# Kernel optimization log

Measured on AMD Instinct MI355X. Metric: run time of the kernel, lower is better.

The kernel has to match this reference:

```python
import jax, jax.numpy as jnp
import numpy as np


def gcn_layer(x, src, dst, deg_inv_sqrt, W, b):
    # PyG GCNConv: h = X W; out[i] = sum_{j->i} norm(j,i) * h[j] + deg_i^{-1} * h[i] + b
    n = x.shape[0]
    h = x @ W                                   # [N, out]
    norm = deg_inv_sqrt[src] * deg_inv_sqrt[dst]  # [E]
    msg = h[src] * norm[:, None]                # [E, out]
    agg = jax.ops.segment_sum(msg, dst, num_segments=n)
    # self-loop contribution (added loops with norm = deg_i^{-1})
    agg = agg + h * (deg_inv_sqrt * deg_inv_sqrt)[:, None]
    return agg + b


def setup_inputs() -> dict:
    key = jax.random.key(0)
    k1, k2, k3, k4, k5, k6 = jax.random.split(key, 6)
    N, E, IN, HID, OUT = 50000, 800000, 128, 128, 64
    x = jax.random.normal(k1, (N, IN), dtype=jnp.float32)
    edge_index = jax.random.randint(k2, (2, E), 0, N, dtype=jnp.int64)
    # glorot-ish init for weights, zeros-ish bias
    W1 = jax.random.normal(k3, (IN, HID), dtype=jnp.float32) * (1.0 / np.sqrt(IN))
    b1 = jax.random.normal(k4, (HID,), dtype=jnp.float32) * 0.01
    W2 = jax.random.normal(k5, (HID, OUT), dtype=jnp.float32) * (1.0 / np.sqrt(HID))
    b2 = jax.random.normal(k6, (OUT,), dtype=jnp.float32) * 0.01
    return {"x": x, "edge_index": edge_index, "W1": W1, "b1": b1, "W2": W2, "b2": b2}


def reference(x, edge_index, W1, b1, W2, b2):
    n = x.shape[0]
    src, dst = edge_index[0], edge_index[1]
    # degree with self-loops (PyG computes degree on the dst/col index)
    deg = jax.ops.segment_sum(jnp.ones_like(dst, dtype=x.dtype), dst, num_segments=n) + 1.0
    deg_inv_sqrt = jax.lax.rsqrt(deg)
    h = gcn_layer(x, src, dst, deg_inv_sqrt, W1, b1)
    h = jax.nn.relu(h)
    # F.dropout with training=False is identity (module evaluated in eval mode)
    out = gcn_layer(h, src, dst, deg_inv_sqrt, W2, b2)
    return out
```

## Files before the change

### kernel.cpp

```cpp
#include <hip/hip_runtime.h>
#include <stdint.h>

typedef __attribute__((ext_vector_type(8))) short short8;
typedef __attribute__((ext_vector_type(4))) float floatx4;

static inline size_t align256(size_t x) { return (x + 255) & ~size_t(255); }

__device__ __forceinline__ unsigned short f2bf(float f) {
    unsigned u = __float_as_uint(f);
    u += 0x7fff + ((u >> 16) & 1);
    return (unsigned short)(u >> 16);
}
__device__ __forceinline__ unsigned pack_bf16(float a, float b) {
    return (unsigned)f2bf(a) | ((unsigned)f2bf(b) << 16);
}
__device__ __forceinline__ float bf_lo(unsigned u) { return __uint_as_float(u << 16); }
__device__ __forceinline__ float bf_hi(unsigned u) { return __uint_as_float(u & 0xffff0000u); }

#define BSHIFT 7
#define NBMAX 1024
#define CH 2048
#define SCAP 3072

__device__ __forceinline__ bool detect_i32(const void* eidx, int E, int t) {
    const long long* e64 = (const long long*)eidx;
    int nchk = E < 256 ? E : 256;
    long long v = e64[t % nchk];
    int bad = (v < 0 || v > 0x7fffffffLL) ? 1 : 0;
    return __syncthreads_or(bad) != 0;
}

__global__ __launch_bounds__(256) void k_hist(const void* __restrict__ eidx, int E,
        int* __restrict__ chist, int NB, int NC,
        const float* __restrict__ W1, const float* __restrict__ W2,
        unsigned short* __restrict__ w1t, unsigned short* __restrict__ w2t,
        int K1, int M1, int K2, int M2) {
    __shared__ int hist[NBMAX];
    const int t = threadIdx.x, B = blockIdx.x;
    if (B < NC) {
        const int e0 = B * CH;
        const int e1 = (e0 + CH < E) ? e0 + CH : E;
        const bool i32 = detect_i32(eidx, E, t);
        const int* e32 = (const int*)eidx;
        const long long* e64 = (const long long*)eidx;
        for (int b0 = 0; b0 < NB; b0 += NBMAX) {
            int bw = (NB - b0 < NBMAX) ? NB - b0 : NBMAX;
            for (int i = t; i < bw; i += 256) hist[i] = 0;
            __syncthreads();
            for (int e = e0 + t; e < e1; e += 256) {
                int d = i32 ? e32[(size_t)E + e] : (int)e64[(size_t)E + e];
                int b = (d >> BSHIFT) - b0;
                if (b >= 0 && b < bw) atomicAdd(&hist[b], 1);
            }
            __syncthreads();
            for (int i = t; i < bw; i += 256) chist[(size_t)(b0 + i) * NC + B] = hist[i];
            __syncthreads();
        }
    } else if (B == NC) {
        for (int j = t; j < K1 * M1; j += 256) {
            int k = j / M1, n = j % M1;
            w1t[(size_t)n * K1 + k] = f2bf(W1[j]);
        }
    } else if (B == NC + 1) {
        for (int j = t; j < K2 * M2; j += 256) {
            int k = j / M2, n = j % M2;
            w2t[(size_t)n * K2 + k] = f2bf(W2[j]);
        }
    }
}

__global__ __launch_bounds__(256) void k_btot(const int* __restrict__ chist,
                                              int* __restrict__ btot, int NB, int NC) {
    int b = blockIdx.x * 4 + (threadIdx.x >> 6);
    if (b >= NB) return;
    int lane = threadIdx.x & 63;
    const int* row = chist + (size_t)b * NC;
    int v = 0;
    for (int i = lane; i < NC; i += 64) v += row[i];
    #pragma unroll
    for (int off = 32; off >= 1; off >>= 1) v += __shfl_xor(v, off, 64);
    if (lane == 0) btot[b] = v;
}

__global__ __launch_bounds__(1024) void k_bscan(const int* __restrict__ btot,
                                                int* __restrict__ bbase,
                                                int* __restrict__ rs_final,
                                                int NB, int N) {
    __shared__ int swt[16];
    const int t = threadIdx.x, lane = t & 63, w = t >> 6;
    int carry = 0;
    for (int base = 0; base < NB; base += 1024) {
        int i = base + t;
        int v = (i < NB) ? btot[i] : 0;
        int incl = v;
        #pragma unroll
        for (int off = 1; off < 64; off <<= 1) {
            int nbr = __shfl_up(incl, off, 64);
            if (lane >= off) incl += nbr;
        }
        if (lane == 63) swt[w] = incl;
        __syncthreads();
        int woff = 0;
        for (int j = 0; j < w; ++j) woff += swt[j];
        if (i < NB) bbase[i] = carry + woff + incl - v;
        int tot = 0;
        for (int j = 0; j < 16; ++j) tot += swt[j];
        carry += tot;
        __syncthreads();
    }
    if (t == 0) { bbase[NB] = carry; rs_final[N] = carry; }
}

__global__ __launch_bounds__(256) void k_hscan2(int* __restrict__ chist,
                                                const int* __restrict__ bbase,
                                                int NB, int NC) {
    int b = blockIdx.x * 4 + (threadIdx.x >> 6);
    if (b >= NB) return;
    int lane = threadIdx.x & 63;
    int* row = chist + (size_t)b * NC;
    int carry = bbase[b];
    for (int base = 0; base < NC; base += 64) {
        int i = base + lane;
        int v = (i < NC) ? row[i] : 0;
        int incl = v;
        #pragma unroll
        for (int off = 1; off < 64; off <<= 1) {
            int nbr = __shfl_up(incl, off, 64);
            if (lane >= off) incl += nbr;
        }
        if (i < NC) row[i] = carry + incl - v;
        carry += __shfl(incl, 63, 64);
    }
}

__global__ __launch_bounds__(256) void k_bfill(const void* __restrict__ eidx, int E,
                                               const int* __restrict__ chist,
                                               uint2* __restrict__ bbuf, int NB, int NC) {
    __shared__ int rank[NBMAX];
    __shared__ int base[NBMAX];
    const int t = threadIdx.x, c = blockIdx.x;
    const int e0 = c * CH;
    const int e1 = (e0 + CH < E) ? e0 + CH : E;
    const bool i32 = detect_i32(eidx, E, t);
    const int* e32 = (const int*)eidx;
    const long long* e64 = (const long long*)eidx;
    for (int b0 = 0; b0 < NB; b0 += NBMAX) {
        int bw = (NB - b0 < NBMAX) ? NB - b0 : NBMAX;
        for (int i = t; i < bw; i += 256) {
            rank[i] = 0;
            base[i] = chist[(size_t)(b0 + i) * NC + c];
        }
        __syncthreads();
        for (int e = e0 + t; e < e1; e += 256) {
            int s, d;
            if (i32) { s = e32[e]; d = e32[(size_t)E + e]; }
            else     { s = (int)e64[e]; d = (int)e64[(size_t)E + e]; }
            int b = (d >> BSHIFT) - b0;
            if (b >= 0 && b < bw) {
                int slot = base[b] + atomicAdd(&rank[b], 1);
                bbuf[slot] = make_uint2((unsigned)s, (unsigned)d);
            }
        }
        __syncthreads();
    }
}

__global__ __launch_bounds__(256) void k_sort(const uint2* __restrict__ bbuf,
                                              const int* __restrict__ bbase,
                                              int* __restrict__ rs_final,
                                              float* __restrict__ dinv,
                                              int* __restrict__ esrc, int N) {
    __shared__ int hist[128];
    __shared__ int off[128];
    __shared__ int srcbuf[SCAP];
    const int b = blockIdx.x, t = threadIdx.x;
    const int node0 = b << BSHIFT;
    const int nloc = (N - node0 < 128) ? N - node0 : 128;
    const int s0 = bbase[b], s1 = bbase[b + 1];
    const int cnt = s1 - s0;
    if (t < 128) hist[t] = 0;
    __syncthreads();
    for (int i = s0 + t; i < s1; i += 256)
        atomicAdd(&hist[bbuf[i].y - (unsigned)node0], 1);
    __syncthreads();
    if (t < 64) {
        int carry = 0;
        #pragma unroll
        for (int base = 0; base < 128; base += 64) {
            int v = hist[base + t];
            int incl = v;
            #pragma unroll
            for (int o = 1; o < 64; o <<= 1) {
                int nbr = __shfl_up(incl, o, 64);
                if (t >= o) incl += nbr;
            }
            off[base + t] = carry + incl - v;
            carry += __shfl(incl, 63, 64);
        }
    }
    __syncthreads();
    if (t < nloc) {
        rs_final[node0 + t] = s0 + off[t];
        dinv[node0 + t] = rsqrtf((float)hist[t] + 1.0f);
    }
    __syncthreads();
    if (t < 128) hist[t] = 0;
    __syncthreads();
    if (cnt <= SCAP) {
        for (int i = s0 + t; i < s1; i += 256) {
            uint2 sd = bbuf[i];
            int lo = sd.y - (unsigned)node0;
            int r = atomicAdd(&hist[lo], 1);
            srcbuf[off[lo] + r] = (int)sd.x;
        }
        __syncthreads();
        for (int i = t; i < cnt; i += 256) esrc[s0 + i] = srcbuf[i];
    } else {
        for (int i = s0 + t; i < s1; i += 256) {
            uint2 sd = bbuf[i];
            int lo = sd.y - (unsigned)node0;
            int r = atomicAdd(&hist[lo], 1);
            esrc[s0 + off[lo] + r] = (int)sd.x;
        }
    }
}

template<int BN, bool AF32>
__global__ __launch_bounds__(256, 3) void k_gemm(
        const void* __restrict__ Av, const unsigned short* __restrict__ Bt,
        const float* __restrict__ dinv, unsigned short* __restrict__ C,
        int N, int M) {
    constexpr int LD = 136;
    __shared__ unsigned short As[64 * LD];
    __shared__ unsigned short Bs[BN * LD];
    const int tid = threadIdx.x;
    const int wave = tid >> 6, lane = tid & 63;
    const int q = lane >> 4, tm = lane & 15;
    const int row0 = blockIdx.x * 64;

    {
        const uint4* Bg = (const uint4*)Bt;
        #pragma unroll
        for (int it = 0; it < BN / 16; ++it) {
            int i = tid + it * 256;
            int r = i >> 4, o = i & 15;
            *(uint4*)&Bs[r * LD + o * 8] = Bg[(size_t)r * 16 + o];
        }
    }
    if (AF32) {
        const float4* Ag = (const float4*)Av;
        #pragma unroll
        for (int it = 0; it < 8; ++it) {
            int i = tid + it * 256;
            int r = i >> 5, o = i & 31;
            int row = row0 + r;
            float4 v = make_float4(0.f, 0.f, 0.f, 0.f);
            if (row < N) v = Ag[(size_t)row * 32 + o];
            uint2 pk;
            pk.x = pack_bf16(v.x, v.y);
            pk.y = pack_bf16(v.z, v.w);
            *(uint2*)&As[r * LD + o * 4] = pk;
        }
    } else {
        const uint4* Ag = (const uint4*)Av;
        #pragma unroll
        for (int it = 0; it < 4; ++it) {
            int i = tid + it * 256;
            int r = i >> 4, o = i & 15;
            int row = row0 + r;
            uint4 v = make_uint4(0, 0, 0, 0);
            if (row < N) v = Ag[(size_t)row * 16 + o];
            *(uint4*)&As[r * LD + o * 8] = v;
        }
    }
    __syncthreads();

    constexpr int NG = BN / 16;
    floatx4 acc[NG];
    #pragma unroll
    for (int g = 0; g < NG; ++g) acc[g] = (floatx4){0.f, 0.f, 0.f, 0.f};

    const int arow = wave * 16 + tm;
    #pragma unroll
    for (int kc = 0; kc < 4; ++kc) {
        short8 af = *(const short8*)&As[arow * LD + kc * 32 + q * 8];
        #pragma unroll
        for (int g = 0; g < NG; ++g) {
            short8 bf = *(const short8*)&Bs[(g * 16 + tm) * LD + kc * 32 + q * 8];
            acc[g] = __builtin_amdgcn_mfma_f32_16x16x32_bf16(af, bf, acc[g], 0, 0, 0);
        }
    }

    float dv[4];
    #pragma unroll
    for (int r = 0; r < 4; ++r) {
        int row = row0 + wave * 16 + q * 4 + r;
        dv[r] = (row < N) ? dinv[row] : 0.f;
    }
    #pragma unroll
    for (int g = 0; g < NG; ++g) {
        #pragma unroll
        for (int r = 0; r < 4; ++r) {
            int row = row0 + wave * 16 + q * 4 + r;
            if (row < N) C[(size_t)row * M + g * 16 + tm] = f2bf(dv[r] * acc[g][r]);
        }
    }
}

__global__ __launch_bounds__(256) void k_agg128(const unsigned* __restrict__ Hb,
        const float* __restrict__ dinv, const int* __restrict__ rs,
        const int* __restrict__ esrc, const float* __restrict__ bias,
        unsigned* __restrict__ out, int N) {
    int wid = (blockIdx.x * 256 + threadIdx.x) >> 6;
    if (wid >= N) return;
    int l = threadIdx.x & 63;
    float di = dinv[wid];
    unsigned a = Hb[(size_t)wid * 64 + l];
    float accx = bf_lo(a), accy = bf_hi(a);
    int k = rs[wid], kend = rs[wid + 1];
    for (; k + 8 <= kend; k += 8) {
        int s[8];
        #pragma unroll
        for (int j = 0; j < 8; ++j) s[j] = esrc[k + j];
        unsigned g[8];
        #pragma unroll
        for (int j = 0; j < 8; ++j) g[j] = Hb[(size_t)s[j] * 64 + l];
        #pragma unroll
        for (int j = 0; j < 8; ++j) { accx += bf_lo(g[j]); accy += bf_hi(g[j]); }
    }
    if (k + 4 <= kend) {
        int s[4];
        #pragma unroll
        for (int j = 0; j < 4; ++j) s[j] = esrc[k + j];
        unsigned g[4];
        #pragma unroll
        for (int j = 0; j < 4; ++j) g[j] = Hb[(size_t)s[j] * 64 + l];
        #pragma unroll
        for (int j = 0; j < 4; ++j) { accx += bf_lo(g[j]); accy += bf_hi(g[j]); }
        k += 4;
    }
    for (; k < kend; ++k) {
        unsigned g = Hb[(size_t)esrc[k] * 64 + l];
        accx += bf_lo(g); accy += bf_hi(g);
    }
    float2 b = ((const float2*)bias)[l];
    float ox = fmaxf(fmaf(di, accx, b.x), 0.f);
    float oy = fmaxf(fmaf(di, accy, b.y), 0.f);
    out[(size_t)wid * 64 + l] = pack_bf16(ox, oy);
}

__global__ __launch_bounds__(256) void k_agg64(const unsigned short* __restrict__ Hb,
        const float* __restrict__ dinv, const int* __restrict__ rs,
        const int* __restrict__ esrc, const float* __restrict__ bias,
        float* __restrict__ out, int N) {
    int wid = (blockIdx.x * 256 + threadIdx.x) >> 6;
    if (wid >= N) return;
    int l = threadIdx.x & 63;
    float di = dinv[wid];
    float acc = __uint_as_float((unsigned)Hb[(size_t)wid * 64 + l] << 16);
    int k = rs[wid], kend = rs[wid + 1];
    for (; k + 8 <= kend; k += 8) {
        int s[8];
        #pragma unroll
        for (int j = 0; j < 8; ++j) s[j] = esrc[k + j];
        unsigned short g[8];
        #pragma unroll
        for (int j = 0; j < 8; ++j) g[j] = Hb[(size_t)s[j] * 64 + l];
        #pragma unroll
        for (int j = 0; j < 8; ++j) acc += __uint_as_float((unsigned)g[j] << 16);
    }
    if (k + 4 <= kend) {
        int s[4];
        #pragma unroll
        for (int j = 0; j < 4; ++j) s[j] = esrc[k + j];
        unsigned short g[4];
        #pragma unroll
        for (int j = 0; j < 4; ++j) g[j] = Hb[(size_t)s[j] * 64 + l];
        #pragma unroll
        for (int j = 0; j < 4; ++j) acc += __uint_as_float((unsigned)g[j] << 16);
        k += 4;
    }
    for (; k < kend; ++k)
        acc += __uint_as_float((unsigned)Hb[(size_t)esrc[k] * 64 + l] << 16);
    out[(size_t)wid * 64 + l] = fmaf(di, acc, bias[l]);
}

extern "C" void kernel_launch(void* const* d_in, const int* in_sizes, int n_in,
                              void* d_out, int out_size, void* d_ws, size_t ws_size,
                              hipStream_t stream) {
    const float* x  = (const float*)d_in[0];
    const void*  ei = d_in[1];
    const float* W1 = (const float*)d_in[2];
    const float* b1 = (const float*)d_in[3];
    const float* W2 = (const float*)d_in[4];
    const float* b2 = (const float*)d_in[5];

    int HID = in_sizes[3];
    int IN  = in_sizes[2] / HID;
    int OUT = in_sizes[4] / HID;
    int N   = in_sizes[0] / IN;
    int E   = in_sizes[1] / 2;
    int NB  = (N + 127) >> BSHIFT;
    int NC  = (E + CH - 1) / CH;

    char* p = (char*)d_ws;
    int* chist     = (int*)p;   p += align256((size_t)NB * NC * 4);
    int* btot      = (int*)p;   p += align256((size_t)NB * 4);
    int* bbase     = (int*)p;   p += align256((size_t)(NB + 1) * 4);
    int* rs_final  = (int*)p;   p += align256((size_t)(N + 1) * 4);
    int* esrc      = (int*)p;   p += align256((size_t)E * 4);
    float* dinv    = (float*)p; p += align256((size_t)N * 4);
    unsigned short* w1t = (unsigned short*)p; p += align256((size_t)HID * IN * 2);
    unsigned short* w2t = (unsigned short*)p; p += align256((size_t)OUT * HID * 2);
    size_t hb_bytes = (size_t)N * HID * 2, bbuf_bytes = (size_t)E * 8;
    uint2* bbuf    = (uint2*)p;
    unsigned short* hb = (unsigned short*)p;
    p += align256(hb_bytes > bbuf_bytes ? hb_bytes : bbuf_bytes);
    unsigned short* h1b = (unsigned short*)p; p += align256((size_t)N * HID * 2);
    unsigned short* h2b = (unsigned short*)p; p += align256((size_t)N * OUT * 2);

    k_hist<<<NC + 2, 256, 0, stream>>>(ei, E, chist, NB, NC,
                                       W1, W2, w1t, w2t, IN, HID, HID, OUT);
    k_btot<<<(NB + 3) / 4, 256, 0, stream>>>(chist, btot, NB, NC);
    k_bscan<<<1, 1024, 0, stream>>>(btot, bbase, rs_final, NB, N);
    k_hscan2<<<(NB + 3) / 4, 256, 0, stream>>>(chist, bbase, NB, NC);
    k_bfill<<<NC, 256, 0, stream>>>(ei, E, chist, bbuf, NB, NC);
    k_sort<<<NB, 256, 0, stream>>>(bbuf, bbase, rs_final, dinv, esrc, N);

    k_gemm<128, true><<<(N + 63) / 64, 256, 0, stream>>>(x, w1t, dinv, hb, N, HID);
    k_agg128<<<(N + 3) / 4, 256, 0, stream>>>((unsigned*)hb, dinv, rs_final, esrc, b1,
                                              (unsigned*)h1b, N);

    k_gemm<64, false><<<(N + 63) / 64, 256, 0, stream>>>(h1b, w2t, dinv, h2b, N, OUT);
    k_agg64<<<(N + 3) / 4, 256, 0, stream>>>(h2b, dinv, rs_final, esrc, b2, (float*)d_out, N);
}
```

Baseline: 208.1 us.

## Split wave into edge sub-groups with 16-byte gathers and fuse block-total scan

The aggregation kernels now split each 64-lane wave into sub-groups that each handle a different edge. Every lane gathers a uint4 of bf16 features, and the partial sums are reduced across sub-groups with xor shuffles. This replaces per-lane 4-byte and 2-byte gathers with 16-byte loads, so more edges are in flight per wave and fewer, wider memory requests are issued. The block-total kernel is also folded into the single-block scan, which removes one launch but serialises the histogram row sums onto one workgroup. The shuffle reduction and masked tail handling add ALU work, and the fused scan assumes NB <= 1024.

```diff
diff --git a/kernel.cpp b/kernel.cpp
--- a/kernel.cpp
+++ b/kernel.cpp
@@ -69,46 +69,39 @@
     }
 }
 
-__global__ __launch_bounds__(256) void k_btot(const int* __restrict__ chist,
-                                              int* __restrict__ btot, int NB, int NC) {
-    int b = blockIdx.x * 4 + (threadIdx.x >> 6);
-    if (b >= NB) return;
-    int lane = threadIdx.x & 63;
-    const int* row = chist + (size_t)b * NC;
-    int v = 0;
-    for (int i = lane; i < NC; i += 64) v += row[i];
-    #pragma unroll
-    for (int off = 32; off >= 1; off >>= 1) v += __shfl_xor(v, off, 64);
-    if (lane == 0) btot[b] = v;
-}
-
-__global__ __launch_bounds__(1024) void k_bscan(const int* __restrict__ btot,
+__global__ __launch_bounds__(1024) void k_bscan(const int* __restrict__ chist,
                                                 int* __restrict__ bbase,
                                                 int* __restrict__ rs_final,
-                                                int NB, int N) {
+                                                int NB, int NC, int N) {
+    __shared__ int tot[1024];
     __shared__ int swt[16];
     const int t = threadIdx.x, lane = t & 63, w = t >> 6;
-    int carry = 0;
-    for (int base = 0; base < NB; base += 1024) {
-        int i = base + t;
-        int v = (i < NB) ? btot[i] : 0;
-        int incl = v;
-        #pragma unroll
-        for (int off = 1; off < 64; off <<= 1) {
-            int nbr = __shfl_up(incl, off, 64);
-            if (lane >= off) incl += nbr;
-        }
-        if (lane == 63) swt[w] = incl;
-        __syncthreads();
-        int woff = 0;
-        for (int j = 0; j < w; ++j) woff += swt[j];
-        if (i < NB) bbase[i] = carry + woff + incl - v;
-        int tot = 0;
-        for (int j = 0; j < 16; ++j) tot += swt[j];
-        carry += tot;
-        __syncthreads();
-    }
-    if (t == 0) { bbase[NB] = carry; rs_final[N] = carry; }
+    for (int b = w; b < NB; b += 16) {
+        const int* row = chist + (size_t)b * NC;
+        int v = 0;
+        for (int i = lane; i < NC; i += 64) v += row[i];
+        #pragma unroll
+        for (int off = 32; off >= 1; off >>= 1) v += __shfl_xor(v, off, 64);
+        if (lane == 0) tot[b] = v;
+    }
+    __syncthreads();
+    int v = (t < NB) ? tot[t] : 0;
+    int incl = v;
+    #pragma unroll
+    for (int off = 1; off < 64; off <<= 1) {
+        int nbr = __shfl_up(incl, off, 64);
+        if (lane >= off) incl += nbr;
+    }
+    if (lane == 63) swt[w] = incl;
+    __syncthreads();
+    int woff = 0;
+    for (int j = 0; j < w; ++j) woff += swt[j];
+    if (t < NB) bbase[t] = woff + incl - v;
+    if (t == 1023) {
+        int total = woff + incl;
+        bbase[NB] = total;
+        rs_final[N] = total;
+    }
 }
 
 __global__ __launch_bounds__(256) void k_hscan2(int* __restrict__ chist,
@@ -307,82 +300,139 @@
     }
 }
 
-__global__ __launch_bounds__(256) void k_agg128(const unsigned* __restrict__ Hb,
+__global__ __launch_bounds__(256) void k_agg128(const uint4* __restrict__ Hv,
         const float* __restrict__ dinv, const int* __restrict__ rs,
         const int* __restrict__ esrc, const float* __restrict__ bias,
-        unsigned* __restrict__ out, int N) {
+        uint4* __restrict__ out, int N) {
     int wid = (blockIdx.x * 256 + threadIdx.x) >> 6;
     if (wid >= N) return;
-    int l = threadIdx.x & 63;
-    float di = dinv[wid];
-    unsigned a = Hb[(size_t)wid * 64 + l];
-    float accx = bf_lo(a), accy = bf_hi(a);
+    const int l = threadIdx.x & 63;
+    const int sub = l >> 4, fl = l & 15;
+    float acc[8];
+    {
+        uint4 a = Hv[(size_t)wid * 16 + fl];
+        float m = (sub == 0) ? 1.f : 0.f;
+        acc[0] = m * bf_lo(a.x); acc[1] = m * bf_hi(a.x);
+        acc[2] = m * bf_lo(a.y); acc[3] = m * bf_hi(a.y);
+        acc[4] = m * bf_lo(a.z); acc[5] = m * bf_hi(a.z);
+        acc[6] = m * bf_lo(a.w); acc[7] = m * bf_hi(a.w);
+    }
     int k = rs[wid], kend = rs[wid + 1];
     for (; k + 8 <= kend; k += 8) {
-        int s[8];
-        #pragma unroll
-        for (int j = 0; j < 8; ++j) s[j] = esrc[k + j];
-        unsigned g[8];
-        #pragma unroll
-        for (int j = 0; j < 8; ++j) g[j] = Hb[(size_t)s[j] * 64 + l];
-        #pragma unroll
-        for (int j = 0; j < 8; ++j) { accx += bf_lo(g[j]); accy += bf_hi(g[j]); }
-    }
-    if (k + 4 <= kend) {
-        int s[4];
-        #pragma unroll
-        for (int j = 0; j < 4; ++j) s[j] = esrc[k + j];
-        unsigned g[4];
-        #pragma unroll
-        for (int j = 0; j < 4; ++j) g[j] = Hb[(size_t)s[j] * 64 + l];
-        #pragma unroll
-        for (int j = 0; j < 4; ++j) { accx += bf_lo(g[j]); accy += bf_hi(g[j]); }
-        k += 4;
-    }
-    for (; k < kend; ++k) {
-        unsigned g = Hb[(size_t)esrc[k] * 64 + l];
-        accx += bf_lo(g); accy += bf_hi(g);
-    }
-    float2 b = ((const float2*)bias)[l];
-    float ox = fmaxf(fmaf(di, accx, b.x), 0.f);
-    float oy = fmaxf(fmaf(di, accy, b.y), 0.f);
-    out[(size_t)wid * 64 + l] = pack_bf16(ox, oy);
-}
-
-__global__ __launch_bounds__(256) void k_agg64(const unsigned short* __restrict__ Hb,
+        int sA = esrc[k + sub];
+        int sB = esrc[k + 4 + sub];
+        uint4 gA = Hv[(size_t)sA * 16 + fl];
+        uint4 gB = Hv[(size_t)sB * 16 + fl];
+        acc[0] += bf_lo(gA.x); acc[1] += bf_hi(gA.x);
+        acc[2] += bf_lo(gA.y); acc[3] += bf_hi(gA.y);
+        acc[4] += bf_lo(gA.z); acc[5] += bf_hi(gA.z);
+        acc[6] += bf_lo(gA.w); acc[7] += bf_hi(gA.w);
+        acc[0] += bf_lo(gB.x); acc[1] += bf_hi(gB.x);
+        acc[2] += bf_lo(gB.y); acc[3] += bf_hi(gB.y);
+        acc[4] += bf_lo(gB.z); acc[5] += bf_hi(gB.z);
+        acc[6] += bf_lo(gB.w); acc[7] += bf_hi(gB.w);
+    }
+    if (k < kend) {
+        int e1 = k + sub, e2 = k + 4 + sub;
+        bool v1 = e1 < kend, v2 = e2 < kend;
+        int sA = v1 ? esrc[e1] : wid;
+        int sB = v2 ? esrc[e2] : wid;
+        uint4 gA = Hv[(size_t)sA * 16 + fl];
+        uint4 gB = Hv[(size_t)sB * 16 + fl];
+        float m1 = v1 ? 1.f : 0.f, m2 = v2 ? 1.f : 0.f;
+        acc[0] = fmaf(m1, bf_lo(gA.x), acc[0]); acc[1] = fmaf(m1, bf_hi(gA.x), acc[1]);
+        acc[2] = fmaf(m1, bf_lo(gA.y), acc[2]); acc[3] = fmaf(m1, bf_hi(gA.y), acc[3]);
+        acc[4] = fmaf(m1, bf_lo(gA.z), acc[4]); acc[5] = fmaf(m1, bf_hi(gA.z), acc[5]);
+        acc[6] = fmaf(m1, bf_lo(gA.w), acc[6]); acc[7] = fmaf(m1, bf_hi(gA.w), acc[7]);
+        acc[0] = fmaf(m2, bf_lo(gB.x), acc[0]); acc[1] = fmaf(m2, bf_hi(gB.x), acc[1]);
+        acc[2] = fmaf(m2, bf_lo(gB.y), acc[2]); acc[3] = fmaf(m2, bf_hi(gB.y), acc[3]);
+        acc[4] = fmaf(m2, bf_lo(gB.z), acc[4]); acc[5] = fmaf(m2, bf_hi(gB.z), acc[5]);
+        acc[6] = fmaf(m2, bf_lo(gB.w), acc[6]); acc[7] = fmaf(m2, bf_hi(gB.w), acc[7]);
+    }
+    #pragma unroll
+    for (int j = 0; j < 8; ++j) {
+        acc[j] += __shfl_xor(acc[j], 16, 64);
+        acc[j] += __shfl_xor(acc[j], 32, 64);
+    }
+    if (sub == 0) {
+        float di = dinv[wid];
+        float4 b0 = ((const float4*)bias)[fl * 2];
+        float4 b1 = ((const float4*)bias)[fl * 2 + 1];
+        uint4 o;
+        o.x = pack_bf16(fmaxf(fmaf(di, acc[0], b0.x), 0.f),
+                        fmaxf(fmaf(di, acc[1], b0.y), 0.f));
+        o.y = pack_bf16(fmaxf(fmaf(di, acc[2], b0.z), 0.f),
+                        fmaxf(fmaf(di, acc[3], b0.w), 0.f));
+        o.z = pack_bf16(fmaxf(fmaf(di, acc[4], b1.x), 0.f),
+                        fmaxf(fmaf(di, acc[5], b1.y), 0.f));
+        o.w = pack_bf16(fmaxf(fmaf(di, acc[6], b1.z), 0.f),
+                        fmaxf(fmaf(di, acc[7], b1.w), 0.f));
+        out[(size_t)wid * 16 + fl] = o;
+    }
+}
+
+__global__ __launch_bounds__(256) void k_agg64(const uint4* __restrict__ Hv,
         const float* __restrict__ dinv, const int* __restrict__ rs,
         const int* __restrict__ esrc, const float* __restrict__ bias,
-        float* __restrict__ out, int N) {
+        float4* __restrict__ out, int N) {
     int wid = (blockIdx.x * 256 + threadIdx.x) >> 6;
     if (wid >= N) return;
-    int l = threadIdx.x & 63;
-    float di = dinv[wid];
-    float acc = __uint_as_float((unsigned)Hb[(size_t)wid * 64 + l] << 16);
+    const int l = threadIdx.x & 63;
+    const int sub = l >> 3, fl = l & 7;
+    float acc[8];
+    {
+        uint4 a = Hv[(size_t)wid * 8 + fl];
+        float m = (sub == 0) ? 1.f : 0.f;
+        acc[0] = m * bf_lo(a.x); acc[1] = m * bf_hi(a.x);
+        acc[2] = m * bf_lo(a.y); acc[3] = m * bf_hi(a.y);
+        acc[4] = m * bf_lo(a.z); acc[5] = m * bf_hi(a.z);
+        acc[6] = m * bf_lo(a.w); acc[7] = m * bf_hi(a.w);
+    }
     int k = rs[wid], kend = rs[wid + 1];
-    for (; k + 8 <= kend; k += 8) {
-        int s[8];
-        #pragma unroll
-        for (int j = 0; j < 8; ++j) s[j] = esrc[k + j];
-        unsigned short g[8];
-        #pragma unroll
-        for (int j = 0; j < 8; ++j) g[j] = Hb[(size_t)s[j] * 64 + l];
-        #pragma unroll
-        for (int j = 0; j < 8; ++j) acc += __uint_as_float((unsigned)g[j] << 16);
-    }
-    if (k + 4 <= kend) {
-        int s[4];
-        #pragma unroll
-        for (int j = 0; j < 4; ++j) s[j] = esrc[k + j];
-        unsigned short g[4];
-        #pragma unroll
-        for (int j = 0; j < 4; ++j) g[j] = Hb[(size_t)s[j] * 64 + l];
-        #pragma unroll
-        for (int j = 0; j < 4; ++j) acc += __uint_as_float((unsigned)g[j] << 16);
-        k += 4;
-    }
-    for (; k < kend; ++k)
-        acc += __uint_as_float((unsigned)Hb[(size_t)esrc[k] * 64 + l] << 16);
-    out[(size_t)wid * 64 + l] = fmaf(di, acc, bias[l]);
+    for (; k + 16 <= kend; k += 16) {
+        int sA = esrc[k + sub];
+        int sB = esrc[k + 8 + sub];
+        uint4 gA = Hv[(size_t)sA * 8 + fl];
+        uint4 gB = Hv[(size_t)sB * 8 + fl];
+        acc[0] += bf_lo(gA.x); acc[1] += bf_hi(gA.x);
+        acc[2] += bf_lo(gA.y); acc[3] += bf_hi(gA.y);
+        acc[4] += bf_lo(gA.z); acc[5] += bf_hi(gA.z);
+        acc[6] += bf_lo(gA.w); acc[7] += bf_hi(gA.w);
+        acc[0] += bf_lo(gB.x); acc[1] += bf_hi(gB.x);
+        acc[2] += bf_lo(gB.y); acc[3] += bf_hi(gB.y);
+        acc[4] += bf_lo(gB.z); acc[5] += bf_hi(gB.z);
+        acc[6] += bf_lo(gB.w); acc[7] += bf_hi(gB.w);
+    }
+    while (k < kend) {
+        int e = k + sub;
+        bool v = e < kend;
+        int s = v ? esrc[e] : wid;
+        uint4 g = Hv[(size_t)s * 8 + fl];
+        float m = v ? 1.f : 0.f;
+        acc[0] = fmaf(m, bf_lo(g.x), acc[0]); acc[1] = fmaf(m, bf_hi(g.x), acc[1]);
+        acc[2] = fmaf(m, bf_lo(g.y), acc[2]); acc[3] = fmaf(m, bf_hi(g.y), acc[3]);
+        acc[4] = fmaf(m, bf_lo(g.z), acc[4]); acc[5] = fmaf(m, bf_hi(g.z), acc[5]);
+        acc[6] = fmaf(m, bf_lo(g.w), acc[6]); acc[7] = fmaf(m, bf_hi(g.w), acc[7]);
+        k += 8;
+    }
+    #pragma unroll
+    for (int j = 0; j < 8; ++j) {
+        acc[j] += __shfl_xor(acc[j], 8, 64);
+        acc[j] += __shfl_xor(acc[j], 16, 64);
+        acc[j] += __shfl_xor(acc[j], 32, 64);
+    }
+    if (sub == 0) {
+        float di = dinv[wid];
+        float4 b0 = ((const float4*)bias)[fl * 2];
+        float4 b1 = ((const float4*)bias)[fl * 2 + 1];
+        float4 o0, o1;
+        o0.x = fmaf(di, acc[0], b0.x); o0.y = fmaf(di, acc[1], b0.y);
+        o0.z = fmaf(di, acc[2], b0.z); o0.w = fmaf(di, acc[3], b0.w);
+        o1.x = fmaf(di, acc[4], b1.x); o1.y = fmaf(di, acc[5], b1.y);
+        o1.z = fmaf(di, acc[6], b1.z); o1.w = fmaf(di, acc[7], b1.w);
+        out[(size_t)wid * 16 + fl * 2]     = o0;
+        out[(size_t)wid * 16 + fl * 2 + 1] = o1;
+    }
 }
 
 extern "C" void kernel_launch(void* const* d_in, const int* in_sizes, int n_in,
@@ -405,7 +455,6 @@
 
     char* p = (char*)d_ws;
     int* chist     = (int*)p;   p += align256((size_t)NB * NC * 4);
-    int* btot      = (int*)p;   p += align256((size_t)NB * 4);
     int* bbase     = (int*)p;   p += align256((size_t)(NB + 1) * 4);
     int* rs_final  = (int*)p;   p += align256((size_t)(N + 1) * 4);
     int* esrc      = (int*)p;   p += align256((size_t)E * 4);
@@ -421,16 +470,16 @@
 
     k_hist<<<NC + 2, 256, 0, stream>>>(ei, E, chist, NB, NC,
                                        W1, W2, w1t, w2t, IN, HID, HID, OUT);
-    k_btot<<<(NB + 3) / 4, 256, 0, stream>>>(chist, btot, NB, NC);
-    k_bscan<<<1, 1024, 0, stream>>>(btot, bbase, rs_final, NB, N);
+    k_bscan<<<1, 1024, 0, stream>>>(chist, bbase, rs_final, NB, NC, N);
     k_hscan2<<<(NB + 3) / 4, 256, 0, stream>>>(chist, bbase, NB, NC);
     k_bfill<<<NC, 256, 0, stream>>>(ei, E, chist, bbuf, NB, NC);
     k_sort<<<NB, 256, 0, stream>>>(bbuf, bbase, rs_final, dinv, esrc, N);
 
     k_gemm<128, true><<<(N + 63) / 64, 256, 0, stream>>>(x, w1t, dinv, hb, N, HID);
-    k_agg128<<<(N + 3) / 4, 256, 0, stream>>>((unsigned*)hb, dinv, rs_final, esrc, b1,
-                                              (unsigned*)h1b, N);
+    k_agg128<<<(N + 3) / 4, 256, 0, stream>>>((const uint4*)hb, dinv, rs_final, esrc, b1,
+                                              (uint4*)h1b, N);
 
     k_gemm<64, false><<<(N + 63) / 64, 256, 0, stream>>>(h1b, w2t, dinv, h2b, N, OUT);
-    k_agg64<<<(N + 3) / 4, 256, 0, stream>>>(h2b, dinv, rs_final, esrc, b2, (float*)d_out, N);
-}
+    k_agg64<<<(N + 3) / 4, 256, 0, stream>>>((const uint4*)h2b, dinv, rs_final, esrc, b2,
+                                             (float4*)d_out, N);
+}
```

Measured after the change: 234.7 us. +12.8%, slower.
